# Performance work log

Measured on AMD Instinct MI355X. Metric: run time of the kernel, lower is better.

The kernel has to match this reference:

```python
import jax, jax.numpy as jnp
import numpy as np

M, K, N, GROUP = 64, 4096, 11008, 128
NGROUPS = K // GROUP  # 32


def setup_inputs() -> dict:
    key = jax.random.key(0)
    k1, k2, k3, k4, k5 = jax.random.split(key, 5)
    x = jax.random.normal(k1, (M, K), dtype=jnp.float32)
    # packed int4 weights: 8 nibbles per int32, full 32-bit entropy
    qweight = jax.random.bits(k2, (K // 8, N), dtype=jnp.uint32).astype(jnp.int32)
    qzeros = jax.random.bits(k3, (NGROUPS, N // 8), dtype=jnp.uint32).astype(jnp.int32)
    scales = jax.random.uniform(k4, (NGROUPS, N), dtype=jnp.float32, minval=0.001, maxval=0.02)
    bias = jax.random.normal(k5, (N,), dtype=jnp.float32) * 0.01
    return {"x": x, "qweight": qweight, "qzeros": qzeros, "scales": scales, "bias": bias}


def dequantize(qweight, qzeros, scales):
    shifts = jnp.arange(8, dtype=jnp.int32) * 4  # nibble bit offsets 0..28
    # unpack weights: [K//8, N] -> [K//8, 8, N] -> [NGROUPS, GROUP, N]
    w = (jnp.right_shift(qweight[:, None, :], shifts[None, :, None]) & 15)
    w = w.reshape(-1, GROUP, qweight.shape[1])
    # unpack zeros: [NGROUPS, N//8] -> [NGROUPS, N//8, 8] -> [NGROUPS, 1, N]; GPTQ stores zero-1
    z = (jnp.right_shift(qzeros[:, :, None], shifts[None, None, :]) & 15) + 1
    z = z.reshape(z.shape[0], 1, -1)
    # scale * (q - zero), per group: [NGROUPS, GROUP, N] -> [K, N]
    W = scales[:, None, :] * (w - z).astype(scales.dtype)
    return W.reshape(-1, W.shape[2])


def reference(x, qweight, qzeros, scales, bias):
    W = dequantize(qweight, qzeros, scales)  # [K, N] fp32
    return jnp.matmul(x, W.astype(x.dtype)) + bias
```

## Files before the change

kernel.cpp:

```cpp
#include <hip/hip_runtime.h>
#include <hip/hip_bf16.h>

namespace {

constexpr int MM = 64;
constexpr int KK = 4096;
constexpr int NN = 11008;
constexpr int NZROW = NN / 8;
constexpr int BN = 128;
constexpr int KSPLIT = 8;
constexpr int KSEG = KK / KSPLIT;
constexpr int NTILES = NN / BN;
constexpr int BK = 32;
constexpr int NCH = KSEG / BK;
constexpr int RS = 20;
constexpr int ABUF = MM * RS;
constexpr int BBUF = BN * RS;
constexpr size_t WS_NEED = (size_t)KSPLIT * MM * NN * 4;

typedef float f32x4 __attribute__((ext_vector_type(4)));
typedef float f32x2 __attribute__((ext_vector_type(2)));
typedef short s16x8 __attribute__((ext_vector_type(8)));
typedef int   i32x4 __attribute__((ext_vector_type(4)));
typedef int   i32x2 __attribute__((ext_vector_type(2)));

__device__ __forceinline__ int pack_bf16(float a, float b) {
  union { __hip_bfloat162 h; int i; } u;
  u.h.x = __float2bfloat16(a);
  u.h.y = __float2bfloat16(b);
  return u.i;
}

__global__ __launch_bounds__(256) void prep_kernel(
    const float* __restrict__ bias, float* __restrict__ out)
{
  const int i = blockIdx.x * 256 + threadIdx.x;
  out[i] = bias[i % NN];
}

__global__ __launch_bounds__(256) void reduce_kernel(
    const float* __restrict__ ws, const float* __restrict__ bias,
    float* __restrict__ out)
{
  const int i4 = (blockIdx.x * 256 + threadIdx.x) * 4;
  f32x4 acc = *(const f32x4*)(bias + (i4 % NN));
  #pragma unroll
  for (int s = 0; s < KSPLIT; ++s)
    acc += *(const f32x4*)(ws + (size_t)s * (MM * NN) + i4);
  *(f32x4*)(out + i4) = acc;
}

template<bool ATOMIC>
__global__ __launch_bounds__(256, 2) void gptq_gemm_kernel(
    const float* __restrict__ x, const int* __restrict__ qw,
    const int* __restrict__ qz, const float* __restrict__ scales,
    float* __restrict__ out)
{
  __shared__ int As[2 * ABUF];
  __shared__ int Bs[2 * BBUF];

  const int tid  = threadIdx.x;
  const int wave = tid >> 6;
  const int lane = tid & 63;
  const int c    = lane & 15;
  const int quad = lane >> 4;

  const int ks     = blockIdx.x & 7;
  const int ntile  = blockIdx.x >> 3;
  const int n0     = ntile * BN;
  const int kbase0 = ks * KSEG;

  const int am   = tid >> 2;
  const int aseg = tid & 3;
  const int bu   = tid & 3;
  const int cp   = tid >> 2;
  const int Ncp  = n0 + 2 * cp;
  const int mrow = wave * 16 + quad * 4;

  const float* xrow = x + am * KK + aseg * 8;

  f32x4 acc[8];
  #pragma unroll
  for (int t = 0; t < 8; ++t) acc[t] = {0.f, 0.f, 0.f, 0.f};

  f32x4 pA0[2], pA1[2];
  i32x2 pB[2];
  f32x2 pS[2];
  int   pZ[2];

  auto pf = [&](int i, int sl) {
    const int kc = kbase0 + i * BK;
    pA0[sl] = *(const f32x4*)(xrow + kc);
    pA1[sl] = *(const f32x4*)(xrow + kc + 4);
    const int g  = kc >> 7;
    const int r0 = kc >> 3;
    pB[sl] = *(const i32x2*)(qw + (size_t)(r0 + bu) * NN + Ncp);
    pS[sl] = *(const f32x2*)(scales + g * NN + Ncp);
    pZ[sl] = qz[g * NZROW + (Ncp >> 3)];
  };

  pf(0, 0);

  #pragma unroll
  for (int i = 0; i < NCH; ++i) {
    const int sl = i & 1;
    if (i + 1 < NCH) pf(i + 1, sl ^ 1);

    int* Abuf = As + sl * ABUF;
    i32x4 pa;
    pa.x = pack_bf16(pA0[sl].x, pA0[sl].y);
    pa.y = pack_bf16(pA0[sl].z, pA0[sl].w);
    pa.z = pack_bf16(pA1[sl].x, pA1[sl].y);
    pa.w = pack_bf16(pA1[sl].z, pA1[sl].w);
    *(i32x4*)&Abuf[am * RS + aseg * 4] = pa;

    int* Bbuf = Bs + sl * BBUF;
    const float s0 = pS[sl].x, s1 = pS[sl].y;
    const int sh0 = (Ncp & 7) * 4;
    const int z0  = (pZ[sl] >> sh0) & 15;
    const int z1  = (pZ[sl] >> (sh0 + 4)) & 15;
    const float C0 = (float)(0x800000 + z0 + 1);
    const float C1 = (float)(0x800000 + z1 + 1);
    const int v0 = pB[sl].x, v1 = pB[sl].y;
    i32x4 pb0, pb1;
    pb0.x = pack_bf16(s0 * (__int_as_float(((v0      ) & 15) | 0x4B000000) - C0),
                      s0 * (__int_as_float(((v0 >>  4) & 15) | 0x4B000000) - C0));
    pb0.y = pack_bf16(s0 * (__int_as_float(((v0 >>  8) & 15) | 0x4B000000) - C0),
                      s0 * (__int_as_float(((v0 >> 12) & 15) | 0x4B000000) - C0));
    pb0.z = pack_bf16(s0 * (__int_as_float(((v0 >> 16) & 15) | 0x4B000000) - C0),
                      s0 * (__int_as_float(((v0 >> 20) & 15) | 0x4B000000) - C0));
    pb0.w = pack_bf16(s0 * (__int_as_float(((v0 >> 24) & 15) | 0x4B000000) - C0),
                      s0 * (__int_as_float(((v0 >> 28) & 15) | 0x4B000000) - C0));
    pb1.x = pack_bf16(s1 * (__int_as_float(((v1      ) & 15) | 0x4B000000) - C1),
                      s1 * (__int_as_float(((v1 >>  4) & 15) | 0x4B000000) - C1));
    pb1.y = pack_bf16(s1 * (__int_as_float(((v1 >>  8) & 15) | 0x4B000000) - C1),
                      s1 * (__int_as_float(((v1 >> 12) & 15) | 0x4B000000) - C1));
    pb1.z = pack_bf16(s1 * (__int_as_float(((v1 >> 16) & 15) | 0x4B000000) - C1),
                      s1 * (__int_as_float(((v1 >> 20) & 15) | 0x4B000000) - C1));
    pb1.w = pack_bf16(s1 * (__int_as_float(((v1 >> 24) & 15) | 0x4B000000) - C1),
                      s1 * (__int_as_float(((v1 >> 28) & 15) | 0x4B000000) - C1));
    *(i32x4*)&Bbuf[(2 * cp    ) * RS + bu * 4] = pb0;
    *(i32x4*)&Bbuf[(2 * cp + 1) * RS + bu * 4] = pb1;

    __asm__ volatile("s_waitcnt lgkmcnt(0)\n\ts_barrier" ::: "memory");

    const s16x8 af = *(const s16x8*)&Abuf[(wave * 16 + c) * RS + quad * 4];
    #pragma unroll
    for (int t = 0; t < 8; ++t) {
      const s16x8 bfr = *(const s16x8*)&Bbuf[(t * 16 + c) * RS + quad * 4];
      acc[t] = __builtin_amdgcn_mfma_f32_16x16x32_bf16(af, bfr, acc[t], 0, 0, 0);
    }
  }

  if (ATOMIC) {
    #pragma unroll
    for (int t = 0; t < 8; ++t) {
      const int N = n0 + t * 16 + c;
      atomicAdd(&out[(mrow + 0) * NN + N], acc[t].x);
      atomicAdd(&out[(mrow + 1) * NN + N], acc[t].y);
      atomicAdd(&out[(mrow + 2) * NN + N], acc[t].z);
      atomicAdd(&out[(mrow + 3) * NN + N], acc[t].w);
    }
  } else {
    float* wsp = out + (size_t)ks * (MM * NN);
    #pragma unroll
    for (int t = 0; t < 8; ++t) {
      const int N = n0 + t * 16 + c;
      wsp[(mrow + 0) * NN + N] = acc[t].x;
      wsp[(mrow + 1) * NN + N] = acc[t].y;
      wsp[(mrow + 2) * NN + N] = acc[t].z;
      wsp[(mrow + 3) * NN + N] = acc[t].w;
    }
  }
}

}

extern "C" void kernel_launch(void* const* d_in, const int* in_sizes, int n_in,
                              void* d_out, int out_size, void* d_ws, size_t ws_size,
                              hipStream_t stream) {
  const float* x      = (const float*)d_in[0];
  const int*   qw     = (const int*)d_in[1];
  const int*   qz     = (const int*)d_in[2];
  const float* scales = (const float*)d_in[3];
  const float* bias   = (const float*)d_in[4];
  float* out = (float*)d_out;

  if (ws_size >= WS_NEED) {
    float* ws = (float*)d_ws;
    gptq_gemm_kernel<false><<<NTILES * KSPLIT, 256, 0, stream>>>(x, qw, qz, scales, ws);
    reduce_kernel<<<(MM * NN) / 1024, 256, 0, stream>>>(ws, bias, out);
  } else {
    prep_kernel<<<(MM * NN) / 256, 256, 0, stream>>>(bias, out);
    gptq_gemm_kernel<true><<<NTILES * KSPLIT, 256, 0, stream>>>(x, qw, qz, scales, out);
  }
}
```

Baseline: 97.22 us.

## Dequantize weights directly into MFMA B fragments in registers, stage only activations

Each wave now owns 32 output columns and dequantizes the packed int4 weights straight into registers laid out as MFMA B operands, so the B tile no longer goes through shared memory. Only x is staged in LDS, in 128-wide K chunks (one quantization group), which removes per-32-K barriers and reloads scales and zeros once per group. The bf16 conversion of weights becomes a byte-permute truncation, and activations use a manual round-to-nearest-even pack. Occupancy is raised to 3 blocks per SM. The cost is weights rounded by truncation instead of RNE, plus higher register pressure from the deeper qweight prefetch.

Measured after the change: 98.03 us. No clear change (+0.8%).

```diff
diff --git a/kernel.cpp b/kernel.cpp
--- a/kernel.cpp
+++ b/kernel.cpp
@@ -11,24 +11,25 @@
 constexpr int KSPLIT = 8;
 constexpr int KSEG = KK / KSPLIT;
 constexpr int NTILES = NN / BN;
-constexpr int BK = 32;
-constexpr int NCH = KSEG / BK;
-constexpr int RS = 20;
-constexpr int ABUF = MM * RS;
-constexpr int BBUF = BN * RS;
+constexpr int SCK = 128;
+constexpr int NSC = KSEG / SCK;
+constexpr int AROW = 68;
+constexpr int ABUF = MM * AROW;
 constexpr size_t WS_NEED = (size_t)KSPLIT * MM * NN * 4;
 
 typedef float f32x4 __attribute__((ext_vector_type(4)));
-typedef float f32x2 __attribute__((ext_vector_type(2)));
 typedef short s16x8 __attribute__((ext_vector_type(8)));
 typedef int   i32x4 __attribute__((ext_vector_type(4)));
-typedef int   i32x2 __attribute__((ext_vector_type(2)));
-
-__device__ __forceinline__ int pack_bf16(float a, float b) {
-  union { __hip_bfloat162 h; int i; } u;
-  u.h.x = __float2bfloat16(a);
-  u.h.y = __float2bfloat16(b);
-  return u.i;
+
+__device__ __forceinline__ int perm_trunc(float even, float odd) {
+  return (int)__builtin_amdgcn_perm(__float_as_uint(odd), __float_as_uint(even), 0x07060302u);
+}
+__device__ __forceinline__ unsigned rne_adj(float f) {
+  unsigned u = __float_as_uint(f);
+  return u + 0x7FFFu + ((u >> 16) & 1u);
+}
+__device__ __forceinline__ int pack_rne(float even, float odd) {
+  return (int)__builtin_amdgcn_perm(rne_adj(odd), rne_adj(even), 0x07060302u);
 }
 
 __global__ __launch_bounds__(256) void prep_kernel(
@@ -51,13 +52,12 @@
 }
 
 template<bool ATOMIC>
-__global__ __launch_bounds__(256, 2) void gptq_gemm_kernel(
+__global__ __launch_bounds__(256, 3) void gptq_gemm_kernel(
     const float* __restrict__ x, const int* __restrict__ qw,
     const int* __restrict__ qz, const float* __restrict__ scales,
     float* __restrict__ out)
 {
-  __shared__ int As[2 * ABUF];
-  __shared__ int Bs[2 * BBUF];
+  __shared__ int Albuf[2 * ABUF];
 
   const int tid  = threadIdx.x;
   const int wave = tid >> 6;
@@ -65,112 +65,152 @@
   const int c    = lane & 15;
   const int quad = lane >> 4;
 
-  const int ks     = blockIdx.x & 7;
-  const int ntile  = blockIdx.x >> 3;
-  const int n0     = ntile * BN;
-  const int kbase0 = ks * KSEG;
-
-  const int am   = tid >> 2;
-  const int aseg = tid & 3;
-  const int bu   = tid & 3;
-  const int cp   = tid >> 2;
-  const int Ncp  = n0 + 2 * cp;
-  const int mrow = wave * 16 + quad * 4;
-
-  const float* xrow = x + am * KK + aseg * 8;
+  const int ks    = blockIdx.x & 7;
+  const int ntile = blockIdx.x >> 3;
+  const int n0    = ntile * BN;
+  const int kbase = ks * KSEG;
+
+  const int sm  = tid >> 2;
+  const int skq = tid & 3;
+  const float* xs = x + sm * KK + kbase + skq * 32;
+
+  const int nb0   = n0 + wave * 32;
+  const int ncol0 = nb0 + c;
+  const int ncol1 = nb0 + 16 + c;
+  const int* qwl  = qw + (size_t)quad * NN + ncol0;
+  const int g0    = ks * NSC;
 
   f32x4 acc[8];
   #pragma unroll
-  for (int t = 0; t < 8; ++t) acc[t] = {0.f, 0.f, 0.f, 0.f};
-
-  f32x4 pA0[2], pA1[2];
-  i32x2 pB[2];
-  f32x2 pS[2];
-  int   pZ[2];
-
-  auto pf = [&](int i, int sl) {
-    const int kc = kbase0 + i * BK;
-    pA0[sl] = *(const f32x4*)(xrow + kc);
-    pA1[sl] = *(const f32x4*)(xrow + kc + 4);
-    const int g  = kc >> 7;
-    const int r0 = kc >> 3;
-    pB[sl] = *(const i32x2*)(qw + (size_t)(r0 + bu) * NN + Ncp);
-    pS[sl] = *(const f32x2*)(scales + g * NN + Ncp);
-    pZ[sl] = qz[g * NZROW + (Ncp >> 3)];
+  for (int i = 0; i < 8; ++i) acc[i] = {0.f, 0.f, 0.f, 0.f};
+
+  f32x4 xv[8];
+  int   qv[4][2];
+  float ps0[2], ps1[2];
+  int   pz0[2], pz1[2];
+
+  auto stage = [&](int sl) {
+    int* Ab = Albuf + sl * ABUF;
+    int iw[16];
+    #pragma unroll
+    for (int j = 0; j < 8; ++j) {
+      iw[2 * j]     = pack_rne(xv[j].x, xv[j].y);
+      iw[2 * j + 1] = pack_rne(xv[j].z, xv[j].w);
+    }
+    #pragma unroll
+    for (int gq = 0; gq < 4; ++gq)
+      *(i32x4*)&Ab[sm * AROW + skq * 16 + gq * 4] = *(const i32x4*)&iw[gq * 4];
   };
 
-  pf(0, 0);
-
-  #pragma unroll
-  for (int i = 0; i < NCH; ++i) {
-    const int sl = i & 1;
-    if (i + 1 < NCH) pf(i + 1, sl ^ 1);
-
-    int* Abuf = As + sl * ABUF;
-    i32x4 pa;
-    pa.x = pack_bf16(pA0[sl].x, pA0[sl].y);
-    pa.y = pack_bf16(pA0[sl].z, pA0[sl].w);
-    pa.z = pack_bf16(pA1[sl].x, pA1[sl].y);
-    pa.w = pack_bf16(pA1[sl].z, pA1[sl].w);
-    *(i32x4*)&Abuf[am * RS + aseg * 4] = pa;
-
-    int* Bbuf = Bs + sl * BBUF;
-    const float s0 = pS[sl].x, s1 = pS[sl].y;
-    const int sh0 = (Ncp & 7) * 4;
-    const int z0  = (pZ[sl] >> sh0) & 15;
-    const int z1  = (pZ[sl] >> (sh0 + 4)) & 15;
-    const float C0 = (float)(0x800000 + z0 + 1);
-    const float C1 = (float)(0x800000 + z1 + 1);
-    const int v0 = pB[sl].x, v1 = pB[sl].y;
-    i32x4 pb0, pb1;
-    pb0.x = pack_bf16(s0 * (__int_as_float(((v0      ) & 15) | 0x4B000000) - C0),
-                      s0 * (__int_as_float(((v0 >>  4) & 15) | 0x4B000000) - C0));
-    pb0.y = pack_bf16(s0 * (__int_as_float(((v0 >>  8) & 15) | 0x4B000000) - C0),
-                      s0 * (__int_as_float(((v0 >> 12) & 15) | 0x4B000000) - C0));
-    pb0.z = pack_bf16(s0 * (__int_as_float(((v0 >> 16) & 15) | 0x4B000000) - C0),
-                      s0 * (__int_as_float(((v0 >> 20) & 15) | 0x4B000000) - C0));
-    pb0.w = pack_bf16(s0 * (__int_as_float(((v0 >> 24) & 15) | 0x4B000000) - C0),
-                      s0 * (__int_as_float(((v0 >> 28) & 15) | 0x4B000000) - C0));
-    pb1.x = pack_bf16(s1 * (__int_as_float(((v1      ) & 15) | 0x4B000000) - C1),
-                      s1 * (__int_as_float(((v1 >>  4) & 15) | 0x4B000000) - C1));
-    pb1.y = pack_bf16(s1 * (__int_as_float(((v1 >>  8) & 15) | 0x4B000000) - C1),
-                      s1 * (__int_as_float(((v1 >> 12) & 15) | 0x4B000000) - C1));
-    pb1.z = pack_bf16(s1 * (__int_as_float(((v1 >> 16) & 15) | 0x4B000000) - C1),
-                      s1 * (__int_as_float(((v1 >> 20) & 15) | 0x4B000000) - C1));
-    pb1.w = pack_bf16(s1 * (__int_as_float(((v1 >> 24) & 15) | 0x4B000000) - C1),
-                      s1 * (__int_as_float(((v1 >> 28) & 15) | 0x4B000000) - C1));
-    *(i32x4*)&Bbuf[(2 * cp    ) * RS + bu * 4] = pb0;
-    *(i32x4*)&Bbuf[(2 * cp + 1) * RS + bu * 4] = pb1;
-
-    __asm__ volatile("s_waitcnt lgkmcnt(0)\n\ts_barrier" ::: "memory");
-
-    const s16x8 af = *(const s16x8*)&Abuf[(wave * 16 + c) * RS + quad * 4];
-    #pragma unroll
-    for (int t = 0; t < 8; ++t) {
-      const s16x8 bfr = *(const s16x8*)&Bbuf[(t * 16 + c) * RS + quad * 4];
-      acc[t] = __builtin_amdgcn_mfma_f32_16x16x32_bf16(af, bfr, acc[t], 0, 0, 0);
+  #pragma unroll
+  for (int j = 0; j < 8; ++j) xv[j] = *(const f32x4*)(xs + j * 4);
+  #pragma unroll
+  for (int ch = 0; ch < 4; ++ch) {
+    const size_t ro = (size_t)(ks * 64 + ch * 4) * NN;
+    qv[ch][0] = qwl[ro];
+    qv[ch][1] = qwl[ro + 16];
+  }
+  ps0[0] = scales[(size_t)g0 * NN + ncol0];
+  ps1[0] = scales[(size_t)g0 * NN + ncol1];
+  pz0[0] = qz[(size_t)g0 * NZROW + (ncol0 >> 3)];
+  pz1[0] = qz[(size_t)g0 * NZROW + (ncol1 >> 3)];
+  stage(0);
+  __asm__ volatile("s_waitcnt lgkmcnt(0)\n\ts_barrier" ::: "memory");
+
+  #pragma unroll
+  for (int s = 0; s < NSC; ++s) {
+    const int sl = s & 1;
+    if (s + 1 < NSC) {
+      #pragma unroll
+      for (int j = 0; j < 8; ++j) xv[j] = *(const f32x4*)(xs + (s + 1) * SCK + j * 4);
+      const int g1 = g0 + s + 1;
+      ps0[(s + 1) & 1] = scales[(size_t)g1 * NN + ncol0];
+      ps1[(s + 1) & 1] = scales[(size_t)g1 * NN + ncol1];
+      pz0[(s + 1) & 1] = qz[(size_t)g1 * NZROW + (ncol0 >> 3)];
+      pz1[(s + 1) & 1] = qz[(size_t)g1 * NZROW + (ncol1 >> 3)];
+    }
+    const float s0v = ps0[sl], s1v = ps1[sl];
+    const float C0 = (float)(0x800000 + ((pz0[sl] >> ((ncol0 & 7) * 4)) & 15) + 1);
+    const float C1 = (float)(0x800000 + ((pz1[sl] >> ((ncol1 & 7) * 4)) & 15) + 1);
+    const int* Ab = Albuf + sl * ABUF;
+
+    #pragma unroll
+    for (int ch = 0; ch < 4; ++ch) {
+      const int v0 = qv[ch][0], v1 = qv[ch][1];
+      if (s + 1 < NSC) {
+        const size_t ro = (size_t)(ks * 64 + (s + 1) * 16 + ch * 4) * NN;
+        qv[ch][0] = qwl[ro];
+        qv[ch][1] = qwl[ro + 16];
+      }
+      i32x4 b0, b1;
+      {
+        const float w0 = s0v * (__int_as_float(((v0      ) & 15) | 0x4B000000) - C0);
+        const float w1 = s0v * (__int_as_float(((v0 >>  4) & 15) | 0x4B000000) - C0);
+        const float w2 = s0v * (__int_as_float(((v0 >>  8) & 15) | 0x4B000000) - C0);
+        const float w3 = s0v * (__int_as_float(((v0 >> 12) & 15) | 0x4B000000) - C0);
+        const float w4 = s0v * (__int_as_float(((v0 >> 16) & 15) | 0x4B000000) - C0);
+        const float w5 = s0v * (__int_as_float(((v0 >> 20) & 15) | 0x4B000000) - C0);
+        const float w6 = s0v * (__int_as_float(((v0 >> 24) & 15) | 0x4B000000) - C0);
+        const float w7 = s0v * (__int_as_float(((v0 >> 28) & 15) | 0x4B000000) - C0);
+        b0.x = perm_trunc(w0, w1); b0.y = perm_trunc(w2, w3);
+        b0.z = perm_trunc(w4, w5); b0.w = perm_trunc(w6, w7);
+      }
+      {
+        const float w0 = s1v * (__int_as_float(((v1      ) & 15) | 0x4B000000) - C1);
+        const float w1 = s1v * (__int_as_float(((v1 >>  4) & 15) | 0x4B000000) - C1);
+        const float w2 = s1v * (__int_as_float(((v1 >>  8) & 15) | 0x4B000000) - C1);
+        const float w3 = s1v * (__int_as_float(((v1 >> 12) & 15) | 0x4B000000) - C1);
+        const float w4 = s1v * (__int_as_float(((v1 >> 16) & 15) | 0x4B000000) - C1);
+        const float w5 = s1v * (__int_as_float(((v1 >> 20) & 15) | 0x4B000000) - C1);
+        const float w6 = s1v * (__int_as_float(((v1 >> 24) & 15) | 0x4B000000) - C1);
+        const float w7 = s1v * (__int_as_float(((v1 >> 28) & 15) | 0x4B000000) - C1);
+        b1.x = perm_trunc(w0, w1); b1.y = perm_trunc(w2, w3);
+        b1.z = perm_trunc(w4, w5); b1.w = perm_trunc(w6, w7);
+      }
+      const s16x8 bf0 = __builtin_bit_cast(s16x8, b0);
+      const s16x8 bf1 = __builtin_bit_cast(s16x8, b1);
+
+      #pragma unroll
+      for (int t = 0; t < 4; ++t) {
+        const s16x8 af = *(const s16x8*)&Ab[(16 * t + c) * AROW + ch * 16 + quad * 4];
+        acc[2 * t]     = __builtin_amdgcn_mfma_f32_16x16x32_bf16(af, bf0, acc[2 * t],     0, 0, 0);
+        acc[2 * t + 1] = __builtin_amdgcn_mfma_f32_16x16x32_bf16(af, bf1, acc[2 * t + 1], 0, 0, 0);
+      }
+    }
+
+    if (s + 1 < NSC) {
+      stage((s + 1) & 1);
+      __asm__ volatile("s_waitcnt lgkmcnt(0)\n\ts_barrier" ::: "memory");
     }
   }
 
   if (ATOMIC) {
     #pragma unroll
-    for (int t = 0; t < 8; ++t) {
-      const int N = n0 + t * 16 + c;
-      atomicAdd(&out[(mrow + 0) * NN + N], acc[t].x);
-      atomicAdd(&out[(mrow + 1) * NN + N], acc[t].y);
-      atomicAdd(&out[(mrow + 2) * NN + N], acc[t].z);
-      atomicAdd(&out[(mrow + 3) * NN + N], acc[t].w);
-    }
+    for (int t = 0; t < 4; ++t)
+      #pragma unroll
+      for (int u = 0; u < 2; ++u) {
+        const int N = nb0 + u * 16 + c;
+        const f32x4 a = acc[2 * t + u];
+        const int m0 = 16 * t + quad * 4;
+        atomicAdd(&out[(m0 + 0) * NN + N], a.x);
+        atomicAdd(&out[(m0 + 1) * NN + N], a.y);
+        atomicAdd(&out[(m0 + 2) * NN + N], a.z);
+        atomicAdd(&out[(m0 + 3) * NN + N], a.w);
+      }
   } else {
     float* wsp = out + (size_t)ks * (MM * NN);
     #pragma unroll
-    for (int t = 0; t < 8; ++t) {
-      const int N = n0 + t * 16 + c;
-      wsp[(mrow + 0) * NN + N] = acc[t].x;
-      wsp[(mrow + 1) * NN + N] = acc[t].y;
-      wsp[(mrow + 2) * NN + N] = acc[t].z;
-      wsp[(mrow + 3) * NN + N] = acc[t].w;
-    }
+    for (int t = 0; t < 4; ++t)
+      #pragma unroll
+      for (int u = 0; u < 2; ++u) {
+        const int N = nb0 + u * 16 + c;
+        const f32x4 a = acc[2 * t + u];
+        const int m0 = 16 * t + quad * 4;
+        wsp[(m0 + 0) * NN + N] = a.x;
+        wsp[(m0 + 1) * NN + N] = a.y;
+        wsp[(m0 + 2) * NN + N] = a.z;
+        wsp[(m0 + 3) * NN + N] = a.w;
+      }
   }
 }
 
```
